# Kernel optimization log

Measured on AMD Instinct MI355X. Metric: run time of the kernel, lower is better.

Reference implementation:

```python
import jax, jax.numpy as jnp
import numpy as np

DIM = 1024
N_HEADS = 8
N_KV_HEADS = 8
Q_C = 128
Q_NOPE = 96
Q_ROPE = 32
KV_C = 128
K_NOPE = 64
K_ROPE = 64
V_HD = 256
EPS = 1e-8
ROPE_THETA = 10000.0


def rms_norm(x, w, eps=EPS):
    return w * x * jax.lax.rsqrt(jnp.mean(x * x, axis=-1, keepdims=True) + eps)


def apply_rope(x, position_ids, head_dim):
    # x: [B, H, S, hd], interleaved even/odd rotation (matches torch module)
    inv_freq = 1.0 / (ROPE_THETA ** (jnp.arange(0, head_dim, 2, dtype=jnp.float32) / head_dim))
    ang = position_ids.astype(jnp.float32)[:, None, :, None] * inv_freq  # [B,1,S,hd/2]
    cos, sin = jnp.cos(ang), jnp.sin(ang)
    xe, xo = x[..., ::2], x[..., 1::2]
    rot = jnp.stack((xe * cos - xo * sin, xe * sin + xo * cos), axis=-1)
    return rot.reshape(x.shape)


def setup_inputs() -> dict:
    key = jax.random.key(0)
    ks = jax.random.split(key, 12)
    B, S = 2, 2048
    s = 0.02
    return {
        "x": jax.random.normal(ks[0], (B, S, DIM), jnp.float32),
        "position_ids": jnp.broadcast_to(jnp.arange(S, dtype=jnp.int32), (B, S)),
        "w_dq_w": jax.random.normal(ks[1], (DIM, Q_C), jnp.float32) * s,
        "w_dq_b": jnp.zeros((Q_C,), jnp.float32),
        "q_norm_w": jnp.ones((Q_C,), jnp.float32),
        "w_uq_qr_w": jax.random.normal(ks[2], (Q_C, N_HEADS * (Q_NOPE + Q_ROPE)), jnp.float32) * s,
        "w_uq_qr_b": jnp.zeros((N_HEADS * (Q_NOPE + Q_ROPE),), jnp.float32),
        "w_dkv_kr_w": jax.random.normal(ks[3], (DIM, KV_C + K_ROPE), jnp.float32) * s,
        "w_dkv_kr_b": jnp.zeros((KV_C + K_ROPE,), jnp.float32),
        "kv_norm_w": jnp.ones((KV_C,), jnp.float32),
        "w_uk_uv_w": jax.random.normal(ks[4], (KV_C, N_KV_HEADS * (K_NOPE + V_HD)), jnp.float32) * s,
        "w_uk_uv_b": jnp.zeros((N_KV_HEADS * (K_NOPE + V_HD),), jnp.float32),
        "w_o_w": jax.random.normal(ks[5], (N_HEADS * V_HD, DIM), jnp.float32) * s,
        "w_o_b": jnp.zeros((DIM,), jnp.float32),
    }


def reference(x, position_ids, w_dq_w, w_dq_b, q_norm_w, w_uq_qr_w, w_uq_qr_b,
              w_dkv_kr_w, w_dkv_kr_b, kv_norm_w, w_uk_uv_w, w_uk_uv_b, w_o_w, w_o_b):
    B, S, _ = x.shape
    # --- Q path: compress -> norm -> up-project, split nope/rope ---
    cq = rms_norm(x @ w_dq_w + w_dq_b, q_norm_w)                     # [B,S,Qc]
    q = cq @ w_uq_qr_w + w_uq_qr_b                                   # [B,S,H*(96+32)]
    q_nope, q_rope = jnp.split(q, [N_HEADS * Q_NOPE], axis=-1)
    q_nope = q_nope.reshape(B, S, N_HEADS, Q_NOPE).transpose(0, 2, 1, 3)
    q_rope = q_rope.reshape(B, S, N_HEADS, Q_ROPE).transpose(0, 2, 1, 3)
    q_rope = apply_rope(q_rope, position_ids, Q_ROPE)
    q_states = jnp.concatenate((q_nope, q_rope), axis=-1)            # [B,H,S,128]
    # --- KV path: compress + shared rope key ---
    ckv_kr = x @ w_dkv_kr_w + w_dkv_kr_b
    ckv, k_rope = jnp.split(ckv_kr, [KV_C], axis=-1)
    ckv = rms_norm(ckv, kv_norm_w)                                   # [B,S,KVc]
    k_rope = apply_rope(k_rope[:, None, :, :], position_ids, K_ROPE) # [B,1,S,64]
    kv = ckv @ w_uk_uv_w + w_uk_uv_b                                 # [B,S,KVh*(64+256)]
    k_nope, v = jnp.split(kv, [N_KV_HEADS * K_NOPE], axis=-1)
    k_nope = k_nope.reshape(B, S, N_KV_HEADS, K_NOPE).transpose(0, 2, 1, 3)
    k_rope = jnp.broadcast_to(k_rope, (B, N_KV_HEADS, S, K_ROPE))
    k_states = jnp.concatenate((k_nope, k_rope), axis=-1)            # [B,KVh,S,128]
    v_states = v.reshape(B, S, N_KV_HEADS, V_HD).transpose(0, 2, 1, 3)
    # gqa_factor = n_heads // n_kv_heads = 1 -> repeat is a no-op
    # --- SDPA (no mask), scale = 1/sqrt(q head dim) ---
    scale = 1.0 / jnp.sqrt(jnp.float32(Q_NOPE + Q_ROPE))
    scores = jnp.einsum("bhqd,bhkd->bhqk", q_states, k_states) * scale
    probs = jax.nn.softmax(scores, axis=-1)
    attn = jnp.einsum("bhqk,bhkd->bhqd", probs, v_states)            # [B,H,S,256]
    attn = attn.transpose(0, 2, 1, 3).reshape(B, S, N_HEADS * V_HD)
    return attn @ w_o_w + w_o_b
```

## Files before the change

### kernel.cpp

```cpp
#include <hip/hip_runtime.h>
#include <hip/hip_bf16.h>
#include <stdint.h>

typedef unsigned short u16;
typedef short short8 __attribute__((ext_vector_type(8)));
typedef float floatx4 __attribute__((ext_vector_type(4)));

#define S_LEN 2048
#define NB 2
#define NH 8
#define R_TOK (NB * S_LEN)

#define L2_THETA 13.287712379549449f
#define QSCALE (0.08838834764831845f * 1.4426950408889634f)

__device__ inline u16 f2bf(float f) {
  union { float f; uint32_t u; } x; x.f = f;
  uint32_t r = (x.u + 0x7fffu + ((x.u >> 16) & 1u)) >> 16;
  return (u16)r;
}
__device__ inline float bf2f(u16 h) {
  union { uint32_t u; float f; } x; x.u = ((uint32_t)h) << 16;
  return x.f;
}
__device__ inline floatx4 mfma16(short8 a, short8 b, floatx4 c) {
  return __builtin_amdgcn_mfma_f32_16x16x32_bf16(a, b, c, 0, 0, 0);
}
__device__ inline uint32_t pkbf(float a, float b) {
  union { __hip_bfloat162 h; uint32_t u; } c;
  c.h = __float22bfloat162_rn(make_float2(a, b));
  return c.u;
}
__device__ __forceinline__ void cp16(const void* g, const void* l) {
  __builtin_amdgcn_global_load_lds(
      (const __attribute__((address_space(1))) uint32_t*)(uintptr_t)g,
      (__attribute__((address_space(3))) uint32_t*)(uintptr_t)l, 16, 0, 0);
}

__global__ __launch_bounds__(256) void k_prep(
    const float* __restrict__ x, u16* __restrict__ xbf,
    const float* __restrict__ wdq, const float* __restrict__ wdkv, u16* __restrict__ waT,
    const float* __restrict__ wuq, u16* __restrict__ wQT,
    const float* __restrict__ wukv, u16* __restrict__ wKVT,
    const float* __restrict__ wo, u16* __restrict__ wOT,
    const float* __restrict__ bdq, const float* __restrict__ bdkv,
    float* __restrict__ biasA) {
  __shared__ u16 tile[32][33];
  const int s = blockIdx.x, tid = threadIdx.x;
  const int tx = tid & 31, ty = tid >> 5;
  if (s < 4096) {
    int i = s * 256 + tid;
    float4 v = ((const float4*)x)[i];
    ushort4 o;
    o.x = f2bf(v.x); o.y = f2bf(v.y); o.z = f2bf(v.z); o.w = f2bf(v.w);
    ((ushort4*)xbf)[i] = o;
  } else if (s < 4416) {
    int t = s - 4096, bx = t % 10, by = t / 10;
    int c0 = bx * 32, r0 = by * 32;
#pragma unroll
    for (int i = 0; i < 4; ++i) {
      int r = r0 + ty + i * 8, c = c0 + tx;
      float v = (c < 128) ? wdq[(size_t)r * 128 + c] : wdkv[(size_t)r * 192 + (c - 128)];
      tile[ty + i * 8][tx] = f2bf(v);
    }
    __syncthreads();
#pragma unroll
    for (int i = 0; i < 4; ++i)
      waT[(size_t)(c0 + ty + i * 8) * 1024 + r0 + tx] = tile[tx][ty + i * 8];
  } else {
    const float* in; u16* out; int R, C, bx, by;
    if (s < 4544) { int t = s - 4416; in = wuq; out = wQT; R = 128; C = 1024; bx = t & 31; by = t >> 5; }
    else if (s < 4864) { int t = s - 4544; in = wukv; out = wKVT; R = 128; C = 2560; bx = t % 80; by = t / 80; }
    else if (s < 6912) { int t = s - 4864; in = wo; out = wOT; R = 2048; C = 1024; bx = t & 31; by = t >> 5; }
    else {
      if (tid < 320) biasA[tid] = (tid < 128) ? bdq[tid] : bdkv[tid - 128];
      return;
    }
    int c0 = bx * 32, r0 = by * 32;
#pragma unroll
    for (int i = 0; i < 4; ++i)
      tile[ty + i * 8][tx] = f2bf(in[(size_t)(r0 + ty + i * 8) * C + c0 + tx]);
    __syncthreads();
#pragma unroll
    for (int i = 0; i < 4; ++i)
      out[(size_t)(c0 + ty + i * 8) * R + r0 + tx] = tile[tx][ty + i * 8];
  }
}

template <int OUT_BF>
__global__ __launch_bounds__(256) void k_gemm_bt(const u16* __restrict__ A,
                                                 const u16* __restrict__ BT,
                                                 const float* __restrict__ bias,
                                                 void* __restrict__ Cout,
                                                 int M, int N, int K) {
  __shared__ __align__(16) u16 Alds[2][128 * 32];
  __shared__ __align__(16) u16 Blds[2][128 * 32];
  const int tid = threadIdx.x;
  const int wave = tid >> 6, lane = tid & 63;
  const int lane15 = lane & 15, quad = lane >> 4;
  const int m0 = blockIdx.y * 128, n0 = blockIdx.x * 128;
  const int mw = (wave & 1) * 64, nw = (wave >> 1) * 64;

  floatx4 acc[4][4];
#pragma unroll
  for (int a = 0; a < 4; ++a)
#pragma unroll
    for (int b = 0; b < 4; ++b) acc[a][b] = (floatx4){0.f, 0.f, 0.f, 0.f};

  const int srow = wave * 32 + (lane >> 2);
  const int scol = (lane & 3) * 8;

  auto stage = [&](int k0, int buf) {
    const u16* ga = A + (size_t)(m0 + srow) * K + k0 + scol;
    cp16(ga, Alds[buf] + srow * 32 + scol);
    cp16(ga + (size_t)16 * K, Alds[buf] + (srow + 16) * 32 + scol);
    const u16* gb = BT + (size_t)(n0 + srow) * K + k0 + scol;
    cp16(gb, Blds[buf] + srow * 32 + scol);
    cp16(gb + (size_t)16 * K, Blds[buf] + (srow + 16) * 32 + scol);
  };

  stage(0, 0);
  int cur = 0;
  for (int k0 = 0; k0 < K; k0 += 32) {
    __syncthreads();
    if (k0 + 32 < K) stage(k0 + 32, cur ^ 1);
    short8 af[4], bf[4];
#pragma unroll
    for (int im = 0; im < 4; ++im)
      af[im] = *(const short8*)&Alds[cur][(mw + im * 16 + lane15) * 32 + quad * 8];
#pragma unroll
    for (int in = 0; in < 4; ++in)
      bf[in] = *(const short8*)&Blds[cur][(nw + in * 16 + lane15) * 32 + quad * 8];
#pragma unroll
    for (int im = 0; im < 4; ++im)
#pragma unroll
      for (int in = 0; in < 4; ++in) acc[im][in] = mfma16(af[im], bf[in], acc[im][in]);
    cur ^= 1;
  }

#pragma unroll
  for (int im = 0; im < 4; ++im)
#pragma unroll
    for (int in = 0; in < 4; ++in)
#pragma unroll
      for (int r = 0; r < 4; ++r) {
        int row = m0 + mw + im * 16 + quad * 4 + r;
        int col = n0 + nw + in * 16 + lane15;
        if (col < N) {
          float v = acc[im][in][r] + bias[col];
          if (OUT_BF)
            ((u16*)Cout)[(size_t)row * N + col] = f2bf(v);
          else
            ((float*)Cout)[(size_t)row * N + col] = v;
        }
      }
}

__global__ void k_stagea(const float* __restrict__ t0, const float* __restrict__ qnw,
                         const float* __restrict__ kvnw, const int* __restrict__ pos_ids,
                         u16* __restrict__ cq, u16* __restrict__ ckv,
                         u16* __restrict__ krope) {
  int r = blockIdx.x, tid = threadIdx.x;
  const float* row = t0 + (size_t)r * 320;
  float a = row[tid];
  float b = row[128 + tid];
  float sa = a * a, sb = b * b;
#pragma unroll
  for (int d = 1; d < 64; d <<= 1) {
    sa += __shfl_xor(sa, d);
    sb += __shfl_xor(sb, d);
  }
  __shared__ float red[4];
  if ((tid & 63) == 0) { red[(tid >> 6) * 2] = sa; red[(tid >> 6) * 2 + 1] = sb; }
  __syncthreads();
  sa = red[0] + red[2];
  sb = red[1] + red[3];
  float ra = rsqrtf(sa * (1.0f / 128.0f) + 1e-8f);
  float rb = rsqrtf(sb * (1.0f / 128.0f) + 1e-8f);
  cq[(size_t)r * 128 + tid] = f2bf(qnw[tid] * a * ra);
  ckv[(size_t)r * 128 + tid] = f2bf(kvnw[tid] * b * rb);
  if (tid < 32) {
    float xe = row[256 + 2 * tid], xo = row[256 + 2 * tid + 1];
    float p = (float)pos_ids[r];
    float freq = exp2f(-(2.0f * tid / 64.0f) * L2_THETA);
    float ang = p * freq;
    float c = cosf(ang), s = sinf(ang);
    krope[(size_t)r * 64 + 2 * tid] = f2bf(xe * c - xo * s);
    krope[(size_t)r * 64 + 2 * tid + 1] = f2bf(xe * s + xo * c);
  }
}

__global__ void k_stageb(const u16* __restrict__ q, const int* __restrict__ pos_ids,
                         u16* __restrict__ qstates) {
  int r = blockIdx.x, tid = threadIdx.x;
  int b = r >> 11, s = r & (S_LEN - 1);
  float p = (float)pos_ids[r];
#pragma unroll
  for (int i = 0; i < 4; ++i) {
    int idx = tid + i * 256;
    int h = idx >> 7, d = idx & 127;
    float val;
    if (d < 96) {
      val = bf2f(q[(size_t)r * 1024 + h * 96 + d]);
    } else {
      int j = d - 96, pr = j >> 1;
      float xe = bf2f(q[(size_t)r * 1024 + 768 + h * 32 + 2 * pr]);
      float xo = bf2f(q[(size_t)r * 1024 + 768 + h * 32 + 2 * pr + 1]);
      float freq = exp2f(-(2.0f * pr / 32.0f) * L2_THETA);
      float ang = p * freq;
      float c = cosf(ang), sn = sinf(ang);
      val = (j & 1) ? (xe * sn + xo * c) : (xe * c - xo * sn);
    }
    qstates[((size_t)(b * NH + h) * S_LEN + s) * 128 + d] = f2bf(val * QSCALE);
  }
}

__global__ __launch_bounds__(256) void k_vt(const u16* __restrict__ kvb, u16* __restrict__ vT) {
  __shared__ u16 tile[64][40];
  const int nx = blockIdx.x;
  const int sy = blockIdx.y;
  const int pz = blockIdx.z;
  const int b = pz >> 3, h = pz & 7;
  const int tid = threadIdx.x;
  const int n0 = nx * 32, s0 = sy * 64;
  {
    int rr = tid >> 2, cc = (tid & 3) * 8;
    const u16* src = kvb + ((size_t)(b * S_LEN + s0 + rr)) * 2560 + 512 + h * 256 + n0 + cc;
    *(short8*)&tile[rr][cc] = *(const short8*)src;
  }
  __syncthreads();
#pragma unroll
  for (int j = 0; j < 2; ++j) {
    int e = tid * 2 + j;
    int n = e >> 4, a = e & 15;
    int sb = 32 * (a >> 3) + 16 * (a & 1) + 4 * ((a >> 1) & 3);
    ushort4 o;
    o.x = tile[sb][n]; o.y = tile[sb + 1][n]; o.z = tile[sb + 2][n]; o.w = tile[sb + 3][n];
    *(ushort4*)&vT[((size_t)(pz * 256 + n0 + n)) * 2048 + s0 + a * 4] = o;
  }
}

__global__ __launch_bounds__(256, 2) void k_attn(const u16* __restrict__ qstates,
                                                 const u16* __restrict__ kv,
                                                 const u16* __restrict__ krope,
                                                 const u16* __restrict__ vT,
                                                 u16* __restrict__ attn_out) {
  const int pair = blockIdx.x;
  const int qblk = blockIdx.y;
  const int b = pair >> 3, h = pair & 7;
  const int tid = threadIdx.x;
  const int wave = tid >> 6, lane = tid & 63;
  const int lane15 = lane & 15, quad = lane >> 4;

  __shared__ __align__(16) u16 Klds[64 * 128];
  __shared__ __align__(16) u16 Vlds[256 * 64];

  const int qrow0 = qblk * 64 + wave * 16;
  short8 qfrag[4];
  {
    const u16* qb = qstates + ((size_t)(b * NH + h) * S_LEN + qrow0 + lane15) * 128 + quad * 8;
#pragma unroll
    for (int c = 0; c < 4; ++c) qfrag[c] = *(const short8*)(qb + c * 32);
  }

  floatx4 o_acc[16];
#pragma unroll
  for (int g = 0; g < 16; ++g) o_acc[g] = (floatx4){0.f, 0.f, 0.f, 0.f};
  float m_i = -1e30f;
  float l_i = 0.f;

  const int kbase = (quad * 16 + lane15) * 8;
  int vo0[4], vo1[4];
#pragma unroll
  for (int ph = 0; ph < 4; ++ph) {
    int n = ph * 16 + lane15;
    int sw = (n ^ (n >> 3)) & 7;
    vo0[ph] = n * 64 + ((quad ^ sw) & 7) * 8;
    vo1[ph] = n * 64 + (((quad | 4) ^ sw) & 7) * 8;
  }

  const int kul = lane >> 4;
  const u16* kp[4];
  int kstr[4];
#pragma unroll
  for (int j = 0; j < 4; ++j) {
    int u = 4 * j + kul;
    const u16* base;
    int str;
    if (u < 8) { base = kv + h * 64 + u * 8; str = 2560; }
    else { base = krope + (u - 8) * 8; str = 64; }
    kp[j] = base + (size_t)(b * S_LEN + wave * 16 + lane15) * str;
    kstr[j] = str;
  }
  auto issueK = [&]() {
#pragma unroll
    for (int j = 0; j < 4; ++j) {
      cp16(kp[j], Klds + ((wave * 16 + 4 * j) * 16 + lane) * 8);
      kp[j] += (size_t)64 * kstr[j];
    }
  };
  const int vn5 = tid >> 3, vsl = tid & 7;
  const u16* vp[8];
#pragma unroll
  for (int oi = 0; oi < 8; ++oi) {
    int n = oi * 32 + vn5;
    int u = vsl ^ ((n ^ (n >> 3)) & 7);
    vp[oi] = vT + ((size_t)pair * 256 + n) * 2048 + u * 8;
  }
  auto issueV = [&]() {
#pragma unroll
    for (int oi = 0; oi < 8; ++oi) {
      cp16(vp[oi], Vlds + ((size_t)(oi * 256 + tid)) * 8);
      vp[oi] += 64;
    }
  };

  issueK();

  for (int ch = 0; ch < S_LEN / 64; ++ch) {
    __syncthreads();
    issueV();

    floatx4 st[4];
#pragma unroll
    for (int t = 0; t < 4; ++t) st[t] = (floatx4){0.f, 0.f, 0.f, 0.f};
    __builtin_amdgcn_s_setprio(1);
#pragma unroll
    for (int c = 0; c < 4; ++c) {
      short8 qf = qfrag[c];
#pragma unroll
      for (int t = 0; t < 4; ++t) {
        short8 kf = *(const short8*)&Klds[kbase + (t * 16 + c * 4) * 128];
        st[t] = mfma16(kf, qf, st[t]);
      }
    }
    __builtin_amdgcn_s_setprio(0);

    float mloc = st[0][0];
#pragma unroll
    for (int t = 0; t < 4; ++t)
#pragma unroll
      for (int r = 0; r < 4; ++r) mloc = fmaxf(mloc, st[t][r]);
    mloc = fmaxf(mloc, __shfl_xor(mloc, 16));
    mloc = fmaxf(mloc, __shfl_xor(mloc, 32));

    const bool resc = __any(mloc > m_i + 8.0f);
    const float mref = resc ? fmaxf(m_i, mloc) : m_i;

    float rs = 0.f;
    union { short8 s; uint4 u; } a01, a23;
    {
      float p0, p1, p2, p3;
      p0 = exp2f(st[0][0] - mref); p1 = exp2f(st[0][1] - mref);
      p2 = exp2f(st[0][2] - mref); p3 = exp2f(st[0][3] - mref);
      rs += (p0 + p1) + (p2 + p3);
      a01.u.x = pkbf(p0, p1); a01.u.y = pkbf(p2, p3);
      p0 = exp2f(st[1][0] - mref); p1 = exp2f(st[1][1] - mref);
      p2 = exp2f(st[1][2] - mref); p3 = exp2f(st[1][3] - mref);
      rs += (p0 + p1) + (p2 + p3);
      a01.u.z = pkbf(p0, p1); a01.u.w = pkbf(p2, p3);
      p0 = exp2f(st[2][0] - mref); p1 = exp2f(st[2][1] - mref);
      p2 = exp2f(st[2][2] - mref); p3 = exp2f(st[2][3] - mref);
      rs += (p0 + p1) + (p2 + p3);
      a23.u.x = pkbf(p0, p1); a23.u.y = pkbf(p2, p3);
      p0 = exp2f(st[3][0] - mref); p1 = exp2f(st[3][1] - mref);
      p2 = exp2f(st[3][2] - mref); p3 = exp2f(st[3][3] - mref);
      rs += (p0 + p1) + (p2 + p3);
      a23.u.z = pkbf(p0, p1); a23.u.w = pkbf(p2, p3);
    }

    if (resc) {
      float alpha = exp2f(m_i - mref);
      m_i = mref;
      l_i = l_i * alpha + rs;
      float al[4];
#pragma unroll
      for (int r = 0; r < 4; ++r) al[r] = __shfl(alpha, quad * 4 + r, 16);
#pragma unroll
      for (int g = 0; g < 16; ++g) {
        o_acc[g][0] *= al[0]; o_acc[g][1] *= al[1];
        o_acc[g][2] *= al[2]; o_acc[g][3] *= al[3];
      }
    } else {
      l_i += rs;
    }

    __syncthreads();
    if (ch + 1 < S_LEN / 64) issueK();

    __builtin_amdgcn_s_setprio(1);
#pragma unroll
    for (int g = 0; g < 16; ++g) {
      short8 b01 = *(const short8*)&Vlds[vo0[g & 3] + (g >> 2) * 4096];
      short8 b23 = *(const short8*)&Vlds[vo1[g & 3] + (g >> 2) * 4096];
      floatx4 o = o_acc[g];
      o = mfma16(a01.s, b01, o);
      o = mfma16(a23.s, b23, o);
      o_acc[g] = o;
    }
    __builtin_amdgcn_s_setprio(0);
  }

  float lsum = l_i;
  lsum += __shfl_xor(lsum, 16);
  lsum += __shfl_xor(lsum, 32);
  float rl = 1.0f / lsum;
  float linv[4];
#pragma unroll
  for (int r = 0; r < 4; ++r) linv[r] = __shfl(rl, quad * 4 + r, 16);
#pragma unroll
  for (int g = 0; g < 16; ++g) {
#pragma unroll
    for (int r = 0; r < 4; ++r) {
      int row = qrow0 + quad * 4 + r;
      int col = h * 256 + g * 16 + lane15;
      attn_out[((size_t)b * S_LEN + row) * 2048 + col] = f2bf(o_acc[g][r] * linv[r]);
    }
  }
}

extern "C" void kernel_launch(void* const* d_in, const int* in_sizes, int n_in,
                              void* d_out, int out_size, void* d_ws, size_t ws_size,
                              hipStream_t stream) {
  const float* x = (const float*)d_in[0];
  const int* pos = (const int*)d_in[1];
  const float* wdq = (const float*)d_in[2];
  const float* bdq = (const float*)d_in[3];
  const float* qnw = (const float*)d_in[4];
  const float* wuq = (const float*)d_in[5];
  const float* buq = (const float*)d_in[6];
  const float* wdkv = (const float*)d_in[7];
  const float* bdkv = (const float*)d_in[8];
  const float* kvnw = (const float*)d_in[9];
  const float* wukv = (const float*)d_in[10];
  const float* bukv = (const float*)d_in[11];
  const float* wo = (const float*)d_in[12];
  const float* bo = (const float*)d_in[13];
  float* out = (float*)d_out;

  char* ws = (char*)d_ws;
  size_t off = 0;
  auto alloc = [&](size_t bytes) {
    char* p = ws + off;
    off += (bytes + 255) & ~(size_t)255;
    return p;
  };
  u16* xbf = (u16*)alloc((size_t)R_TOK * 1024 * 2);
  float* t0 = (float*)alloc((size_t)R_TOK * 320 * 4);
  u16* qout = (u16*)alloc((size_t)R_TOK * 1024 * 2);
  u16* vT = (u16*)d_ws;
  u16* waT = (u16*)alloc((size_t)384 * 1024 * 2);
  float* biasA = (float*)alloc(320 * 4);
  u16* wQT = (u16*)alloc((size_t)1024 * 128 * 2);
  u16* wKVT = (u16*)alloc((size_t)2560 * 128 * 2);
  u16* wOT = (u16*)alloc((size_t)1024 * 2048 * 2);
  u16* cq = (u16*)alloc((size_t)R_TOK * 128 * 2);
  u16* ckv = (u16*)alloc((size_t)R_TOK * 128 * 2);
  u16* krope = (u16*)alloc((size_t)R_TOK * 64 * 2);
  u16* qst = (u16*)alloc((size_t)R_TOK * 1024 * 2);
  u16* kvb = (u16*)alloc((size_t)R_TOK * 2560 * 2);
  u16* attnb = (u16*)alloc((size_t)R_TOK * 2048 * 2);
  (void)ws_size; (void)n_in; (void)in_sizes; (void)out_size;

  k_prep<<<6913, 256, 0, stream>>>(x, xbf, wdq, wdkv, waT, wuq, wQT, wukv, wKVT, wo, wOT,
                                   bdq, bdkv, biasA);

  k_gemm_bt<0><<<dim3(3, 32), 256, 0, stream>>>(xbf, waT, biasA, t0, R_TOK, 320, 1024);
  k_stagea<<<R_TOK, 128, 0, stream>>>(t0, qnw, kvnw, pos, cq, ckv, krope);
  k_gemm_bt<1><<<dim3(8, 32), 256, 0, stream>>>(cq, wQT, buq, qout, R_TOK, 1024, 128);
  k_stageb<<<R_TOK, 256, 0, stream>>>(qout, pos, qst);
  k_gemm_bt<1><<<dim3(20, 32), 256, 0, stream>>>(ckv, wKVT, bukv, kvb, R_TOK, 2560, 128);
  k_vt<<<dim3(8, 32, 16), 256, 0, stream>>>(kvb, vT);
  k_attn<<<dim3(16, 32), 256, 0, stream>>>(qst, kvb, krope, vT, attnb);
  k_gemm_bt<0><<<dim3(8, 32), 256, 0, stream>>>(attnb, wOT, bo, out, R_TOK, 1024, 2048);
}
```

Before: 276.1 us.

## Double-buffer K/V tiles in attention with 8-wave blocks sharing loads

```diff
diff --git a/kernel.cpp b/kernel.cpp
--- a/kernel.cpp
+++ b/kernel.cpp
@@ -240,22 +240,23 @@
   }
 }
 
-__global__ __launch_bounds__(256, 2) void k_attn(const u16* __restrict__ qstates,
-                                                 const u16* __restrict__ kv,
-                                                 const u16* __restrict__ krope,
-                                                 const u16* __restrict__ vT,
-                                                 u16* __restrict__ attn_out) {
+__global__ __launch_bounds__(512) void k_attn(const u16* __restrict__ qstates,
+                                              const u16* __restrict__ kv,
+                                              const u16* __restrict__ krope,
+                                              const u16* __restrict__ vT,
+                                              u16* __restrict__ attn_out) {
   const int pair = blockIdx.x;
   const int qblk = blockIdx.y;
   const int b = pair >> 3, h = pair & 7;
   const int tid = threadIdx.x;
   const int wave = tid >> 6, lane = tid & 63;
   const int lane15 = lane & 15, quad = lane >> 4;
-
-  __shared__ __align__(16) u16 Klds[64 * 128];
-  __shared__ __align__(16) u16 Vlds[256 * 64];
-
-  const int qrow0 = qblk * 64 + wave * 16;
+  const int w4 = wave & 3, half = wave >> 2;
+
+  __shared__ __align__(16) u16 Klds[2][64 * 128];
+  __shared__ __align__(16) u16 Vlds[2][256 * 64];
+
+  const int qrow0 = qblk * 128 + wave * 16;
   short8 qfrag[4];
   {
     const u16* qb = qstates + ((size_t)(b * NH + h) * S_LEN + qrow0 + lane15) * 128 + quad * 8;
@@ -279,47 +280,56 @@
     vo1[ph] = n * 64 + (((quad | 4) ^ sw) & 7) * 8;
   }
 
-  const int kul = lane >> 4;
-  const u16* kp[4];
-  int kstr[4];
-#pragma unroll
-  for (int j = 0; j < 4; ++j) {
-    int u = 4 * j + kul;
+  const u16* kp[2];
+  int kstr[2];
+  int kdst[2];
+#pragma unroll
+  for (int j = 0; j < 2; ++j) {
+    int u = half * 8 + j * 4 + quad;
     const u16* base;
     int str;
     if (u < 8) { base = kv + h * 64 + u * 8; str = 2560; }
     else { base = krope + (u - 8) * 8; str = 64; }
-    kp[j] = base + (size_t)(b * S_LEN + wave * 16 + lane15) * str;
+    kp[j] = base + (size_t)(b * S_LEN + w4 * 16 + lane15) * str;
     kstr[j] = str;
-  }
-  auto issueK = [&]() {
-#pragma unroll
-    for (int j = 0; j < 4; ++j) {
-      cp16(kp[j], Klds + ((wave * 16 + 4 * j) * 16 + lane) * 8);
-      kp[j] += (size_t)64 * kstr[j];
-    }
-  };
-  const int vn5 = tid >> 3, vsl = tid & 7;
-  const u16* vp[8];
-#pragma unroll
-  for (int oi = 0; oi < 8; ++oi) {
-    int n = oi * 32 + vn5;
+    kdst[j] = (w4 * 256 + (half * 2 + j) * 64 + lane) * 8;
+  }
+  const int vn6 = tid >> 3, vsl = tid & 7;
+  const u16* vp[4];
+#pragma unroll
+  for (int oi = 0; oi < 4; ++oi) {
+    int n = oi * 64 + vn6;
     int u = vsl ^ ((n ^ (n >> 3)) & 7);
     vp[oi] = vT + ((size_t)pair * 256 + n) * 2048 + u * 8;
   }
-  auto issueV = [&]() {
-#pragma unroll
-    for (int oi = 0; oi < 8; ++oi) {
-      cp16(vp[oi], Vlds + ((size_t)(oi * 256 + tid)) * 8);
+
+  auto issueK = [&](int buf) {
+#pragma unroll
+    for (int j = 0; j < 2; ++j) {
+      cp16(kp[j], &Klds[buf][kdst[j]]);
+      kp[j] += (size_t)64 * kstr[j];
+    }
+  };
+  auto issueV = [&](int buf) {
+#pragma unroll
+    for (int oi = 0; oi < 4; ++oi) {
+      cp16(vp[oi], &Vlds[buf][(oi * 512 + tid) * 8]);
       vp[oi] += 64;
     }
   };
 
-  issueK();
-
+  issueK(0);
+  issueV(0);
+  asm volatile("s_waitcnt vmcnt(0)" ::: "memory");
+  __builtin_amdgcn_sched_barrier(0);
+  __builtin_amdgcn_s_barrier();
+
+  int cur = 0;
   for (int ch = 0; ch < S_LEN / 64; ++ch) {
-    __syncthreads();
-    issueV();
+    if (ch + 1 < S_LEN / 64) {
+      issueK(cur ^ 1);
+      issueV(cur ^ 1);
+    }
 
     floatx4 st[4];
 #pragma unroll
@@ -330,7 +340,7 @@
       short8 qf = qfrag[c];
 #pragma unroll
       for (int t = 0; t < 4; ++t) {
-        short8 kf = *(const short8*)&Klds[kbase + (t * 16 + c * 4) * 128];
+        short8 kf = *(const short8*)&Klds[cur][kbase + (t * 16 + c * 4) * 128];
         st[t] = mfma16(kf, qf, st[t]);
       }
     }
@@ -385,20 +395,22 @@
       l_i += rs;
     }
 
-    __syncthreads();
-    if (ch + 1 < S_LEN / 64) issueK();
-
     __builtin_amdgcn_s_setprio(1);
 #pragma unroll
     for (int g = 0; g < 16; ++g) {
-      short8 b01 = *(const short8*)&Vlds[vo0[g & 3] + (g >> 2) * 4096];
-      short8 b23 = *(const short8*)&Vlds[vo1[g & 3] + (g >> 2) * 4096];
+      short8 b01 = *(const short8*)&Vlds[cur][vo0[g & 3] + (g >> 2) * 4096];
+      short8 b23 = *(const short8*)&Vlds[cur][vo1[g & 3] + (g >> 2) * 4096];
       floatx4 o = o_acc[g];
       o = mfma16(a01.s, b01, o);
       o = mfma16(a23.s, b23, o);
       o_acc[g] = o;
     }
     __builtin_amdgcn_s_setprio(0);
+
+    asm volatile("s_waitcnt vmcnt(0)" ::: "memory");
+    __builtin_amdgcn_sched_barrier(0);
+    __builtin_amdgcn_s_barrier();
+    cur ^= 1;
   }
 
   float lsum = l_i;
@@ -471,6 +483,6 @@
   k_stageb<<<R_TOK, 256, 0, stream>>>(qout, pos, qst);
   k_gemm_bt<1><<<dim3(20, 32), 256, 0, stream>>>(ckv, wKVT, bukv, kvb, R_TOK, 2560, 128);
   k_vt<<<dim3(8, 32, 16), 256, 0, stream>>>(kvb, vT);
-  k_attn<<<dim3(16, 32), 256, 0, stream>>>(qst, kvb, krope, vT, attnb);
+  k_attn<<<dim3(16, 16), 512, 0, stream>>>(qst, kvb, krope, vT, attnb);
   k_gemm_bt<0><<<dim3(8, 32), 256, 0, stream>>>(attnb, wOT, bo, out, R_TOK, 1024, 2048);
 }
```

Measured after the change: 275.0 us. About the same (-0.4%).
